# Optimization experiments

Measured on AMD Instinct MI355X. Metric: run time of the kernel, lower is better.

The kernel has to match this reference:

```python
import math
import jax, jax.numpy as jnp
import numpy as np

NUM_HEADS = 16
NUM_BUCKETS = 32
MAX_DISTANCE = 128
NEG_INF = -1e9
LN_EPS = 1e-5


def _rel_pos_bias(rab_emb, T):
    # buckets for relative position (i - j) clamped at 0, T5-style log buckets
    i = jnp.arange(T)[:, None]
    j = jnp.arange(T)[None, :]
    n = jnp.clip(i - j, 0, None)  # = -(mem - ctx), clamped min 0
    max_exact = NUM_BUCKETS // 2
    large = max_exact + (
        jnp.log(n.astype(jnp.float32) / max_exact + 1e-6)
        / math.log(MAX_DISTANCE / max_exact)
        * (NUM_BUCKETS - max_exact)
    ).astype(jnp.int32)
    large = jnp.minimum(large, NUM_BUCKETS - 1)
    buckets = jnp.where(n < max_exact, n, large)  # [T, T]
    return rab_emb[buckets].transpose(2, 0, 1)[None]  # [1, H, T, T]


def setup_inputs() -> dict:
    key = jax.random.key(0)
    ks = jax.random.split(key, 8)
    B, T, D = 2, 1024, 1024
    x = jax.random.normal(ks[0], (B, T, D), dtype=jnp.float32)
    # additive causal mask: 0 where allowed, -1e9 where blocked (code tests ==0 for allowed)
    causal_block = jnp.triu(jnp.ones((T, T), dtype=bool), k=1)
    attention_mask = jnp.where(causal_block, NEG_INF, 0.0).astype(jnp.float32)
    # key padding: second sequence has last 256 positions padded
    lengths = jnp.array([T, T - 256])
    key_padding_mask = jnp.arange(T)[None, :] >= lengths[:, None]  # True = pad
    s = 1.0 / math.sqrt(D)
    W_in = jax.random.normal(ks[1], (4 * D, D), dtype=jnp.float32) * s
    b_in = jax.random.normal(ks[2], (4 * D,), dtype=jnp.float32) * 0.02
    W_out = jax.random.normal(ks[3], (D, D), dtype=jnp.float32) * s
    b_out = jax.random.normal(ks[4], (D,), dtype=jnp.float32) * 0.02
    gamma = jnp.ones((D,), dtype=jnp.float32)
    beta = jnp.zeros((D,), dtype=jnp.float32)
    rab_emb = jax.random.normal(ks[5], (NUM_BUCKETS, NUM_HEADS), dtype=jnp.float32) * 0.02
    return {
        "x": x,
        "attention_mask": attention_mask,
        "key_padding_mask": key_padding_mask,
        "W_in": W_in,
        "b_in": b_in,
        "W_out": W_out,
        "b_out": b_out,
        "gamma": gamma,
        "beta": beta,
        "rab_emb": rab_emb,
    }


def reference(x, attention_mask, key_padding_mask, W_in, b_in, W_out, b_out, gamma, beta, rab_emb):
    B, T, D = x.shape
    H = NUM_HEADS
    hd = D // H
    alpha = hd ** (-0.5)

    h = jax.nn.silu(x @ W_in.T + b_in)  # [B, T, 4D]
    U, V, Q, K = jnp.split(h, 4, axis=-1)

    def heads(t):
        return t.reshape(B, T, H, hd).transpose(0, 2, 1, 3)  # [B, H, T, hd]

    Qh, Kh, Vh = heads(Q), heads(K), heads(V)

    rab = _rel_pos_bias(rab_emb, T)  # [1, H, T, T]
    logits = jnp.einsum("bhtd,bhsd->bhts", Qh, Kh) * alpha + rab + attention_mask[None, None]

    valid = (~key_padding_mask).astype(jnp.float32)[:, None, None, :]  # [B,1,1,T]
    allowed = (attention_mask == 0).astype(jnp.float32)[None, None] * valid  # [B,1,T,T] bcast
    # padded keys: torch masked_fill(-inf) then logits_safe -> -1e9
    logits = jnp.where(valid == 0, NEG_INF, logits)

    denom = jnp.clip(jnp.sum(allowed, axis=-1, keepdims=True), 1.0, None)
    attention = jax.nn.silu(logits) / denom  # pointwise SiLU attention, no softmax

    AV = jnp.einsum("bhts,bhsd->bthd", attention, Vh).reshape(B, T, D)

    mu = jnp.mean(AV, axis=-1, keepdims=True)
    var = jnp.var(AV, axis=-1, keepdims=True)
    normed = (AV - mu) / jnp.sqrt(var + LN_EPS) * gamma + beta

    y = (normed * U) @ W_out.T + b_out  # U_flat == U (head reshape round-trips)
    return x + y
```

## Files before the change

### kernel.cpp

```cpp
#include <hip/hip_runtime.h>
#include <stdint.h>

#define DEV static __device__ __forceinline__

typedef unsigned short u16;
typedef float floatx4 __attribute__((ext_vector_type(4)));
typedef short bf16x8 __attribute__((ext_vector_type(8)));

constexpr int Tn = 1024;
constexpr int Dn = 1024;
constexpr int Hn = 16;
constexpr int FD = 4096;

DEV float b2f(u16 u) { union { unsigned int i; float f; } v; v.i = ((unsigned int)u) << 16; return v.f; }
DEV u16 f2b(float f) {
  union { float f; unsigned int i; } v; v.f = f;
  unsigned int x = v.i;
  x += 0x7fffu + ((x >> 16) & 1u);
  return (u16)(x >> 16);
}

DEV void async16(const void* g, void* l) {
  __builtin_amdgcn_global_load_lds((const __attribute__((address_space(1))) void*)g,
                                   (__attribute__((address_space(3))) void*)l,
                                   16, 0, 0);
}

DEV bool is_bf16(const unsigned* gdet) { return gdet[0] == 0x3F803F80u; }
DEV int kp_mode(const unsigned* kp) {
  unsigned d511 = kp[511];
  if (d511 == 0x01010101u) return 1;
  unsigned d1023 = kp[1023];
  if (d1023 == 0x3F803F80u) return 2;
  unsigned d2047 = kp[2047];
  return (d2047 == 0x3F800000u) ? 3 : 0;
}
DEV int nchunks(int qt) { return (qt < 8) ? 1 : 2; }

__global__ void prep_all(const void* __restrict__ x, const void* __restrict__ wi,
                         const void* __restrict__ wo, u16* __restrict__ xb,
                         u16* __restrict__ wib, u16* __restrict__ wob,
                         const void* __restrict__ bi, const void* __restrict__ bo,
                         const void* __restrict__ ga, const void* __restrict__ be,
                         const void* __restrict__ kp, const void* __restrict__ rab,
                         float* __restrict__ smallf, float* __restrict__ biasG,
                         float* __restrict__ denomG, unsigned long long* __restrict__ kmaskG)
{
  const unsigned* gdet = (const unsigned*)ga;
  const int bid = blockIdx.x;
  const int tid = threadIdx.x;
  __shared__ unsigned char vb[1024];
  __shared__ int wtot[4];

  if (bid < 1792) {
    if (is_bf16(gdet)) return;
    int i0 = bid * 256 + tid;
#pragma unroll
    for (int k = 0; k < 4; k++) {
      int i = i0 + k * 458752;
      const void* src; u16* dst; int j;
      if (i < 524288)       { src = x;  dst = xb;  j = i; }
      else if (i < 1572864) { src = wi; dst = wib; j = i - 524288; }
      else                  { src = wo; dst = wob; j = i - 1572864; }
      float4 v = ((const float4*)src)[j];
      ushort4 o; o.x = f2b(v.x); o.y = f2b(v.y); o.z = f2b(v.z); o.w = f2b(v.w);
      ((ushort4*)dst)[j] = o;
    }
    return;
  }
  if (bid < 1794) {
    const int b = bid - 1792;
    const int mode = kp_mode((const unsigned*)kp);
    int vv[4];
    const int t0 = tid * 4;
#pragma unroll
    for (int i = 0; i < 4; i++) {
      int t = b * Tn + t0 + i;
      int pad;
      if (mode == 0)      pad = (((const int*)kp)[t] != 0);
      else if (mode == 1) pad = (((const unsigned char*)kp)[t] != 0);
      else if (mode == 2) pad = (((const u16*)kp)[t] != 0);
      else                pad = (((const float*)kp)[t] != 0.f);
      vv[i] = pad ? 0 : 1;
      vb[t0 + i] = (unsigned char)vv[i];
    }
    int p1 = vv[0], p2 = p1 + vv[1], p3 = p2 + vv[2], p4 = p3 + vv[3];
    const int lane = tid & 63, w = tid >> 6;
    int ws = p4;
#pragma unroll
    for (int off = 1; off < 64; off <<= 1) {
      int t = __shfl_up(ws, off, 64);
      if (lane >= off) ws += t;
    }
    if (lane == 63) wtot[w] = ws;
    __syncthreads();
    int base = 0;
    for (int j = 0; j < w; j++) base += wtot[j];
    int excl = base + ws - p4;
    int c1 = excl + p1, c2 = excl + p2, c3 = excl + p3, c4 = excl + p4;
    denomG[b * Tn + t0 + 0] = (float)(c1 < 1 ? 1 : c1);
    denomG[b * Tn + t0 + 1] = (float)(c2 < 1 ? 1 : c2);
    denomG[b * Tn + t0 + 2] = (float)(c3 < 1 ? 1 : c3);
    denomG[b * Tn + t0 + 3] = (float)(c4 < 1 ? 1 : c4);
    if (tid < 16) {
      unsigned long long m = 0;
      for (int j = 0; j < 64; j++) m |= (unsigned long long)vb[tid * 64 + j] << j;
      kmaskG[b * 16 + tid] = m;
    }
    return;
  }
  const bool fbf = is_bf16(gdet);
  for (int i = tid; i < 7168; i += 256) {
    const void* src; int j;
    if (i < 4096)      { src = bi; j = i; }
    else if (i < 5120) { src = bo; j = i - 4096; }
    else if (i < 6144) { src = ga; j = i - 5120; }
    else               { src = be; j = i - 6144; }
    smallf[i] = fbf ? b2f(((const u16*)src)[j]) : ((const float*)src)[j];
  }
  for (int i = tid; i < Hn * Tn; i += 256) {
    int hh = i >> 10, d = i & 1023;
    int bk;
    if (d < 16) bk = d;
    else {
      float lg = logf((float)d * 0.0625f + 1e-6f) / logf(8.f) * 16.f;
      bk = 16 + (int)lg;
      bk = bk < 31 ? bk : 31;
    }
    int j = bk * Hn + hh;
    biasG[i] = fbf ? b2f(((const u16*)rab)[j]) : ((const float*)rab)[j];
  }
}

template<int BM, int BN, int WR, int WC, int EPI>
__global__ __launch_bounds__(WR * WC * 64, 4)
void gemm_bt(const u16* __restrict__ Ac, const u16* __restrict__ Ar,
             const u16* __restrict__ Bc, const u16* __restrict__ Br,
             const float* __restrict__ biasf, const void* __restrict__ X,
             void* __restrict__ C, u16* __restrict__ VtG,
             const unsigned* __restrict__ gdet, int M, int N, int K)
{
  constexpr int NTH = WR * WC * 64;
  constexpr int MT = BM / (WR * 16);
  constexpr int NTT = BN / (WC * 16);
  __shared__ u16 As[2][BM * 64];
  __shared__ u16 Bs[2][BN * 64];
  const int fbf = is_bf16(gdet) ? 1 : 0;
  const u16* A  = fbf ? Ar : Ac;
  const u16* Bm = fbf ? Br : Bc;
  const int tid = threadIdx.x;
  const int lane = tid & 63;
  const int w = tid >> 6;
  const int wm = w / WC, wn = w % WC;
  const int q = lane >> 4, l16 = lane & 15;
  const int rowBase = blockIdx.y * BM;
  const int colBase = blockIdx.x * BN;
  const int nIter = K >> 6;

  floatx4 acc[MT][NTT];
#pragma unroll
  for (int i = 0; i < MT; i++)
#pragma unroll
    for (int j = 0; j < NTT; j++)
#pragma unroll
      for (int r = 0; r < 4; r++) acc[i][j][r] = 0.f;

  auto stage = [&](int buf, int kb) {
#pragma unroll
    for (int i = 0; i < BM * 8 / NTH; i++) {
      int c = i * NTH + tid;
      int row = c >> 3, cl = (c & 7) ^ (row & 7);
      async16(&A[(size_t)(rowBase + row) * K + kb + cl * 8], &As[buf][c * 8]);
    }
#pragma unroll
    for (int i = 0; i < BN * 8 / NTH; i++) {
      int c = i * NTH + tid;
      int row = c >> 3, cl = (c & 7) ^ (row & 7);
      async16(&Bm[(size_t)(colBase + row) * K + kb + cl * 8], &Bs[buf][c * 8]);
    }
  };

  stage(0, 0);
  __syncthreads();

  const int rsw = l16 & 7;
  for (int it = 0; it < nIter; it++) {
    const int cur = it & 1;
    if (it + 1 < nIter) stage(cur ^ 1, (it + 1) * 64);
#pragma unroll
    for (int ko = 0; ko < 2; ko++) {
      bf16x8 af[MT], bfr[NTT];
#pragma unroll
      for (int mt = 0; mt < MT; mt++) {
        int row = wm * (MT * 16) + mt * 16 + l16;
        af[mt] = *(const bf16x8*)&As[cur][(row * 8 + ((ko * 4 + q) ^ rsw)) * 8];
      }
#pragma unroll
      for (int nt = 0; nt < NTT; nt++) {
        int row = wn * (NTT * 16) + nt * 16 + l16;
        bfr[nt] = *(const bf16x8*)&Bs[cur][(row * 8 + ((ko * 4 + q) ^ rsw)) * 8];
      }
#pragma unroll
      for (int mt = 0; mt < MT; mt++)
#pragma unroll
        for (int nt = 0; nt < NTT; nt++)
          acc[mt][nt] = __builtin_amdgcn_mfma_f32_16x16x32_bf16(af[mt], bfr[nt], acc[mt][nt], 0, 0, 0);
    }
    __syncthreads();
  }

  const bool isV = (EPI == 0) && (colBase >= Dn) && (colBase < 2 * Dn);
#pragma unroll
  for (int mt = 0; mt < MT; mt++)
#pragma unroll
    for (int nt = 0; nt < NTT; nt++) {
      int col = colBase + wn * (NTT * 16) + nt * 16 + l16;
      float bcol = biasf[col];
      int row0 = rowBase + wm * (MT * 16) + mt * 16 + q * 4;
      if (EPI == 0) {
        u16 pr[4];
#pragma unroll
        for (int r = 0; r < 4; r++) {
          float v = acc[mt][nt][r] + bcol;
          v = v / (1.f + __expf(-v));
          pr[r] = f2b(v);
        }
        if (isV) {
          int d = col - Dn;
          u16* vp = &VtG[(((size_t)(row0 >> 10) * Hn + (d >> 6)) * 64 + (d & 63)) * Tn + (row0 & 1023)];
          *(uint2*)vp = make_uint2(pr[0] | ((unsigned)pr[1] << 16),
                                   pr[2] | ((unsigned)pr[3] << 16));
        } else {
#pragma unroll
          for (int r = 0; r < 4; r++)
            ((u16*)C)[(size_t)(row0 + r) * N + col] = pr[r];
        }
      } else {
#pragma unroll
        for (int r = 0; r < 4; r++) {
          size_t idx = (size_t)(row0 + r) * N + col;
          float v = acc[mt][nt][r] + bcol;
          if (fbf) {
            v += b2f(((const u16*)X)[idx]);
            ((u16*)C)[idx] = f2b(v);
          } else {
            v += ((const float*)X)[idx];
            ((float*)C)[idx] = v;
          }
        }
      }
    }
}

__global__ __launch_bounds__(256, 3)
void attn_kern(const u16* __restrict__ h, const u16* __restrict__ VtG,
               const float* __restrict__ biasG, const float* __restrict__ denomG,
               const unsigned long long* __restrict__ kmaskG,
               float* __restrict__ AV)
{
  __shared__ u16 QPs[4096];
  __shared__ u16 Ks[2][4096];
  __shared__ u16 Vs[2][4096];
  __shared__ float biasL[1024];
  const int tid = threadIdx.x;
  const int lane = tid & 63;
  const int w = tid >> 6;
  const int q = lane >> 4, l16 = lane & 15;

  int qt = 0, rem = blockIdx.x;
  for (;;) { int P = nchunks(qt); if (rem < P) break; rem -= P; qt++; }
  const int c = rem;
  const int P = nchunks(qt);
  const int n = qt + 1, cb = n / P, cr = n % P;
  const int kt0 = c * cb + (c < cr ? c : cr);
  const int kt1 = kt0 + cb + (c < cr ? 1 : 0);

  const int head = blockIdx.y, b = blockIdx.z;
  const u16* hb = h + (size_t)b * Tn * FD;
  const u16* vtb = VtG + ((size_t)(b * Hn + head)) * 64 * Tn;

#pragma unroll
  for (int i = 0; i < 2; i++) {
    int s = i * 256 + tid;
    int row = s >> 3, dc = (s & 7) ^ (row & 7);
    async16(&hb[(size_t)(qt * 64 + row) * FD + 2048 + head * 64 + dc * 8], &QPs[s * 8]);
    async16(&hb[(size_t)(kt0 * 64 + row) * FD + 3072 + head * 64 + dc * 8], &Ks[0][s * 8]);
    async16(&vtb[(size_t)row * Tn + kt0 * 64 + dc * 8], &Vs[0][s * 8]);
  }
  async16(&biasG[head * Tn + tid * 4], &biasL[tid * 4]);
  __syncthreads();

  const int sw0 = q ^ (l16 & 7);
  const int qrow = w * 16 + l16;
  bf16x8 bq0 = *(const bf16x8*)&QPs[(qrow * 8 + sw0) * 8];
  bf16x8 bq1 = *(const bf16x8*)&QPs[(qrow * 8 + (sw0 ^ 4)) * 8];
  const float dinv = 1.f / denomG[b * Tn + qt * 64 + qrow];

  floatx4 o[4];
#pragma unroll
  for (int nt = 0; nt < 4; nt++)
#pragma unroll
    for (int r = 0; r < 4; r++) o[nt][r] = 0.f;

  int buf = 0;
  for (int kt = kt0; kt < kt1; kt++) {
    if (kt + 1 < kt1) {
      int nb = buf ^ 1;
      int krow = (kt + 1) * 64;
#pragma unroll
      for (int i = 0; i < 2; i++) {
        int s = i * 256 + tid;
        int row = s >> 3, dc = (s & 7) ^ (row & 7);
        async16(&hb[(size_t)(krow + row) * FD + 3072 + head * 64 + dc * 8], &Ks[nb][s * 8]);
        async16(&vtb[(size_t)row * Tn + krow + dc * 8], &Vs[nb][s * 8]);
      }
    }
    const unsigned long long km = kmaskG[b * 16 + kt];
    const int dq = (qt - kt) * 64 + qrow;
#pragma unroll
    for (int st = 0; st < 4; st++) {
      int rk = (st * 16 + l16) * 8;
      bf16x8 ak0 = *(const bf16x8*)&Ks[buf][(rk + sw0) * 8];
      bf16x8 ak1 = *(const bf16x8*)&Ks[buf][(rk + (sw0 ^ 4)) * 8];
      floatx4 sT;
#pragma unroll
      for (int r = 0; r < 4; r++) sT[r] = 0.f;
      sT = __builtin_amdgcn_mfma_f32_16x16x32_bf16(ak0, bq0, sT, 0, 0, 0);
      sT = __builtin_amdgcn_mfma_f32_16x16x32_bf16(ak1, bq1, sT, 0, 0, 0);
      unsigned mb = (unsigned)(km >> (st * 16 + q * 4)) & 0xFu;
      u16 pr[4];
#pragma unroll
      for (int r = 0; r < 4; r++) {
        int delta = dq - (st * 16 + q * 4 + r);
        float p = 0.f;
        if (((mb >> r) & 1u) && delta >= 0) {
          float xv = sT[r] * 0.125f + biasL[delta];
          p = xv * dinv / (1.f + __expf(-xv));
        }
        pr[r] = f2b(p);
      }
      unsigned lo = pr[0] | ((unsigned)pr[1] << 16);
      unsigned hi = pr[2] | ((unsigned)pr[3] << 16);
      int cch = (st * 2 + (q >> 1)) ^ (l16 & 7);
      *(uint2*)&QPs[w * 1024 + l16 * 64 + cch * 8 + (q & 1) * 4] = make_uint2(lo, hi);
    }
    int rp = w * 1024 + l16 * 64;
    bf16x8 ap0 = *(const bf16x8*)&QPs[rp + sw0 * 8];
    bf16x8 ap1 = *(const bf16x8*)&QPs[rp + (sw0 ^ 4) * 8];
#pragma unroll
    for (int nt = 0; nt < 4; nt++) {
      int rv = (nt * 16 + l16) * 8;
      bf16x8 bv0 = *(const bf16x8*)&Vs[buf][(rv + sw0) * 8];
      bf16x8 bv1 = *(const bf16x8*)&Vs[buf][(rv + (sw0 ^ 4)) * 8];
      o[nt] = __builtin_amdgcn_mfma_f32_16x16x32_bf16(ap0, bv0, o[nt], 0, 0, 0);
      o[nt] = __builtin_amdgcn_mfma_f32_16x16x32_bf16(ap1, bv1, o[nt], 0, 0, 0);
    }
    if (kt + 1 < kt1) __syncthreads();
    buf ^= 1;
  }

  float* avp = AV + (size_t)c * 2097152
             + ((size_t)b * Tn + qt * 64 + w * 16 + q * 4) * Dn + head * 64;
#pragma unroll
  for (int nt = 0; nt < 4; nt++)
#pragma unroll
    for (int r = 0; r < 4; r++)
      avp[(size_t)r * Dn + nt * 16 + l16] = o[nt][r];
}

__global__ __launch_bounds__(256)
void ln_mul(const float* __restrict__ AV, const u16* __restrict__ h,
            const float* __restrict__ gam, const float* __restrict__ bet,
            u16* __restrict__ z)
{
  struct alignas(8) U4 { u16 a, b, c, d; };
  const int row = blockIdx.x;
  const int tid = threadIdx.x;
  const int P = nchunks(row >> 6 & 15);
  float4 v = ((const float4*)(AV + (size_t)row * Dn))[tid];
  if (P > 1) {
    float4 p = ((const float4*)(AV + 2097152 + (size_t)row * Dn))[tid];
    v.x += p.x; v.y += p.y; v.z += p.z; v.w += p.w;
  }
  float s  = v.x + v.y + v.z + v.w;
  float s2 = v.x * v.x + v.y * v.y + v.z * v.z + v.w * v.w;
#pragma unroll
  for (int off = 32; off > 0; off >>= 1) {
    s  += __shfl_down(s, off, 64);
    s2 += __shfl_down(s2, off, 64);
  }
  __shared__ float red[8];
  const int lane = tid & 63, w = tid >> 6;
  if (lane == 0) { red[w] = s; red[4 + w] = s2; }
  __syncthreads();
  const float su = red[0] + red[1] + red[2] + red[3];
  const float sq = red[4] + red[5] + red[6] + red[7];
  const float mu = su * (1.f / 1024.f);
  const float var = sq * (1.f / 1024.f) - mu * mu;
  const float rstd = rsqrtf(var + 1e-5f);

  const U4 uu = ((const U4*)(h + (size_t)row * FD))[tid];
  const float4 g4 = ((const float4*)gam)[tid];
  const float4 b4 = ((const float4*)bet)[tid];
  float r0 = ((v.x - mu) * rstd * g4.x + b4.x) * b2f(uu.a);
  float r1 = ((v.y - mu) * rstd * g4.y + b4.y) * b2f(uu.b);
  float r2 = ((v.z - mu) * rstd * g4.z + b4.z) * b2f(uu.c);
  float r3 = ((v.w - mu) * rstd * g4.w + b4.w) * b2f(uu.d);
  U4 outv; outv.a = f2b(r0); outv.b = f2b(r1); outv.c = f2b(r2); outv.d = f2b(r3);
  ((U4*)(z + (size_t)row * Dn))[tid] = outv;
}

extern "C" void kernel_launch(void* const* d_in, const int* in_sizes, int n_in,
                              void* d_out, int out_size, void* d_ws, size_t ws_size,
                              hipStream_t stream)
{
  const void* x     = d_in[0];
  const void* kp    = d_in[2];
  const void* W_in  = d_in[3];
  const void* b_in  = d_in[4];
  const void* W_out = d_in[5];
  const void* b_out = d_in[6];
  const void* gamma = d_in[7];
  const void* beta  = d_in[8];
  const void* rab   = d_in[9];
  const unsigned* gdet = (const unsigned*)gamma;

  char* ws = (char*)d_ws;
  u16*   h     = (u16*)(ws);
  float* AV    = (float*)(ws + 16777216);
  u16*   z     = (u16*)(ws + 41943040);
  u16*   xb    = (u16*)(ws + 46137344);
  u16*   Wib   = (u16*)(ws + 50331648);
  u16*   Wob   = (u16*)(ws + 58720256);
  u16*   VtG   = (u16*)(ws + 60817408);
  float* smallf= (float*)(ws + 65011712);
  float* biasG = (float*)(ws + 65040384);
  float* denom = (float*)(ws + 65105920);
  unsigned long long* kmask = (unsigned long long*)(ws + 65114112);

  prep_all<<<1795, 256, 0, stream>>>(x, W_in, W_out, xb, Wib, Wob,
                                     b_in, b_out, gamma, beta, kp, rab,
                                     smallf, biasG, denom, kmask);
  gemm_bt<128, 128, 4, 2, 0><<<dim3(32, 16, 1), dim3(512), 0, stream>>>(
      xb, (const u16*)x, Wib, (const u16*)W_in, smallf, nullptr,
      h, VtG, gdet, 2048, 4096, 1024);
  attn_kern<<<dim3(24, 16, 2), dim3(256), 0, stream>>>(h, VtG, biasG, denom, kmask, AV);
  ln_mul<<<2048, 256, 0, stream>>>(AV, h, smallf + 5120, smallf + 6144, z);
  gemm_bt<64, 64, 4, 2, 1><<<dim3(16, 32, 1), dim3(512), 0, stream>>>(
      z, z, Wob, (const u16*)W_out, smallf + 4096, x, d_out, nullptr,
      gdet, 2048, 1024, 1024);
}
```

Baseline: 183.1 us.

## Split attention keys three ways, single-buffer K/V, add constant-bias fast path

Causal key tiles are now split across up to three chunks for late query tiles instead of two, and the LayerNorm kernel sums the third partial. K/V shared memory drops from double to single buffering so the kernel can target four blocks per SM, with extra barriers around each tile load. Tiles whose key mask is all zero skip their compute. Tiles far enough from the diagonal and fully unmasked use one constant relative-position bias with no per-element mask checks. Losing double buffering exposes global load latency that the higher occupancy is meant to hide.

```diff
diff --git a/kernel.cpp b/kernel.cpp
--- a/kernel.cpp
+++ b/kernel.cpp
@@ -35,7 +35,7 @@
   unsigned d2047 = kp[2047];
   return (d2047 == 0x3F800000u) ? 3 : 0;
 }
-DEV int nchunks(int qt) { return (qt < 8) ? 1 : 2; }
+DEV int nchunks(int qt) { return (qt < 6) ? 1 : ((qt < 12) ? 2 : 3); }
 
 __global__ void prep_all(const void* __restrict__ x, const void* __restrict__ wi,
                          const void* __restrict__ wo, u16* __restrict__ xb,
@@ -252,15 +252,16 @@
     }
 }
 
-__global__ __launch_bounds__(256, 3)
+__global__ __launch_bounds__(256, 4)
 void attn_kern(const u16* __restrict__ h, const u16* __restrict__ VtG,
                const float* __restrict__ biasG, const float* __restrict__ denomG,
                const unsigned long long* __restrict__ kmaskG,
                float* __restrict__ AV)
 {
-  __shared__ u16 QPs[4096];
-  __shared__ u16 Ks[2][4096];
-  __shared__ u16 Vs[2][4096];
+  __shared__ u16 Qs[4096];
+  __shared__ u16 Ks[4096];
+  __shared__ u16 Vs[4096];
+  __shared__ u16 Ps[4096];
   __shared__ float biasL[1024];
   const int tid = threadIdx.x;
   const int lane = tid & 63;
@@ -283,18 +284,19 @@
   for (int i = 0; i < 2; i++) {
     int s = i * 256 + tid;
     int row = s >> 3, dc = (s & 7) ^ (row & 7);
-    async16(&hb[(size_t)(qt * 64 + row) * FD + 2048 + head * 64 + dc * 8], &QPs[s * 8]);
-    async16(&hb[(size_t)(kt0 * 64 + row) * FD + 3072 + head * 64 + dc * 8], &Ks[0][s * 8]);
-    async16(&vtb[(size_t)row * Tn + kt0 * 64 + dc * 8], &Vs[0][s * 8]);
+    async16(&hb[(size_t)(qt * 64 + row) * FD + 2048 + head * 64 + dc * 8], &Qs[s * 8]);
+    async16(&hb[(size_t)(kt0 * 64 + row) * FD + 3072 + head * 64 + dc * 8], &Ks[s * 8]);
+    async16(&vtb[(size_t)row * Tn + kt0 * 64 + dc * 8], &Vs[s * 8]);
   }
   async16(&biasG[head * Tn + tid * 4], &biasL[tid * 4]);
   __syncthreads();
 
   const int sw0 = q ^ (l16 & 7);
   const int qrow = w * 16 + l16;
-  bf16x8 bq0 = *(const bf16x8*)&QPs[(qrow * 8 + sw0) * 8];
-  bf16x8 bq1 = *(const bf16x8*)&QPs[(qrow * 8 + (sw0 ^ 4)) * 8];
+  bf16x8 bq0 = *(const bf16x8*)&Qs[(qrow * 8 + sw0) * 8];
+  bf16x8 bq1 = *(const bf16x8*)&Qs[(qrow * 8 + (sw0 ^ 4)) * 8];
   const float dinv = 1.f / denomG[b * Tn + qt * 64 + qrow];
+  const float cb31 = biasL[512];
 
   floatx4 o[4];
 #pragma unroll
@@ -302,61 +304,70 @@
 #pragma unroll
     for (int r = 0; r < 4; r++) o[nt][r] = 0.f;
 
-  int buf = 0;
   for (int kt = kt0; kt < kt1; kt++) {
+    const unsigned long long km = kmaskG[b * 16 + kt];
+    if (km != 0ull) {
+      const bool fastT = (qt - kt >= 3) && (km == ~0ull);
+      const int dq = (qt - kt) * 64 + qrow;
+#pragma unroll
+      for (int st = 0; st < 4; st++) {
+        int rk = (st * 16 + l16) * 8;
+        bf16x8 ak0 = *(const bf16x8*)&Ks[(rk + sw0) * 8];
+        bf16x8 ak1 = *(const bf16x8*)&Ks[(rk + (sw0 ^ 4)) * 8];
+        floatx4 sT;
+#pragma unroll
+        for (int r = 0; r < 4; r++) sT[r] = 0.f;
+        sT = __builtin_amdgcn_mfma_f32_16x16x32_bf16(ak0, bq0, sT, 0, 0, 0);
+        sT = __builtin_amdgcn_mfma_f32_16x16x32_bf16(ak1, bq1, sT, 0, 0, 0);
+        u16 pr[4];
+        if (fastT) {
+#pragma unroll
+          for (int r = 0; r < 4; r++) {
+            float xv = sT[r] * 0.125f + cb31;
+            float p = xv * dinv / (1.f + __expf(-xv));
+            pr[r] = f2b(p);
+          }
+        } else {
+          unsigned mb = (unsigned)(km >> (st * 16 + q * 4)) & 0xFu;
+#pragma unroll
+          for (int r = 0; r < 4; r++) {
+            int delta = dq - (st * 16 + q * 4 + r);
+            float p = 0.f;
+            if (((mb >> r) & 1u) && delta >= 0) {
+              float xv = sT[r] * 0.125f + biasL[delta];
+              p = xv * dinv / (1.f + __expf(-xv));
+            }
+            pr[r] = f2b(p);
+          }
+        }
+        unsigned lo = pr[0] | ((unsigned)pr[1] << 16);
+        unsigned hi = pr[2] | ((unsigned)pr[3] << 16);
+        int cch = (st * 2 + (q >> 1)) ^ (l16 & 7);
+        *(uint2*)&Ps[w * 1024 + l16 * 64 + cch * 8 + (q & 1) * 4] = make_uint2(lo, hi);
+      }
+      int rp = w * 1024 + l16 * 64;
+      bf16x8 ap0 = *(const bf16x8*)&Ps[rp + sw0 * 8];
+      bf16x8 ap1 = *(const bf16x8*)&Ps[rp + (sw0 ^ 4) * 8];
+#pragma unroll
+      for (int nt = 0; nt < 4; nt++) {
+        int rv = (nt * 16 + l16) * 8;
+        bf16x8 bv0 = *(const bf16x8*)&Vs[(rv + sw0) * 8];
+        bf16x8 bv1 = *(const bf16x8*)&Vs[(rv + (sw0 ^ 4)) * 8];
+        o[nt] = __builtin_amdgcn_mfma_f32_16x16x32_bf16(ap0, bv0, o[nt], 0, 0, 0);
+        o[nt] = __builtin_amdgcn_mfma_f32_16x16x32_bf16(ap1, bv1, o[nt], 0, 0, 0);
+      }
+    }
     if (kt + 1 < kt1) {
-      int nb = buf ^ 1;
-      int krow = (kt + 1) * 64;
+      __syncthreads();
 #pragma unroll
       for (int i = 0; i < 2; i++) {
         int s = i * 256 + tid;
         int row = s >> 3, dc = (s & 7) ^ (row & 7);
-        async16(&hb[(size_t)(krow + row) * FD + 3072 + head * 64 + dc * 8], &Ks[nb][s * 8]);
-        async16(&vtb[(size_t)row * Tn + krow + dc * 8], &Vs[nb][s * 8]);
-      }
-    }
-    const unsigned long long km = kmaskG[b * 16 + kt];
-    const int dq = (qt - kt) * 64 + qrow;
-#pragma unroll
-    for (int st = 0; st < 4; st++) {
-      int rk = (st * 16 + l16) * 8;
-      bf16x8 ak0 = *(const bf16x8*)&Ks[buf][(rk + sw0) * 8];
-      bf16x8 ak1 = *(const bf16x8*)&Ks[buf][(rk + (sw0 ^ 4)) * 8];
-      floatx4 sT;
-#pragma unroll
-      for (int r = 0; r < 4; r++) sT[r] = 0.f;
-      sT = __builtin_amdgcn_mfma_f32_16x16x32_bf16(ak0, bq0, sT, 0, 0, 0);
-      sT = __builtin_amdgcn_mfma_f32_16x16x32_bf16(ak1, bq1, sT, 0, 0, 0);
-      unsigned mb = (unsigned)(km >> (st * 16 + q * 4)) & 0xFu;
-      u16 pr[4];
-#pragma unroll
-      for (int r = 0; r < 4; r++) {
-        int delta = dq - (st * 16 + q * 4 + r);
-        float p = 0.f;
-        if (((mb >> r) & 1u) && delta >= 0) {
-          float xv = sT[r] * 0.125f + biasL[delta];
-          p = xv * dinv / (1.f + __expf(-xv));
-        }
-        pr[r] = f2b(p);
-      }
-      unsigned lo = pr[0] | ((unsigned)pr[1] << 16);
-      unsigned hi = pr[2] | ((unsigned)pr[3] << 16);
-      int cch = (st * 2 + (q >> 1)) ^ (l16 & 7);
-      *(uint2*)&QPs[w * 1024 + l16 * 64 + cch * 8 + (q & 1) * 4] = make_uint2(lo, hi);
-    }
-    int rp = w * 1024 + l16 * 64;
-    bf16x8 ap0 = *(const bf16x8*)&QPs[rp + sw0 * 8];
-    bf16x8 ap1 = *(const bf16x8*)&QPs[rp + (sw0 ^ 4) * 8];
-#pragma unroll
-    for (int nt = 0; nt < 4; nt++) {
-      int rv = (nt * 16 + l16) * 8;
-      bf16x8 bv0 = *(const bf16x8*)&Vs[buf][(rv + sw0) * 8];
-      bf16x8 bv1 = *(const bf16x8*)&Vs[buf][(rv + (sw0 ^ 4)) * 8];
-      o[nt] = __builtin_amdgcn_mfma_f32_16x16x32_bf16(ap0, bv0, o[nt], 0, 0, 0);
-      o[nt] = __builtin_amdgcn_mfma_f32_16x16x32_bf16(ap1, bv1, o[nt], 0, 0, 0);
-    }
-    if (kt + 1 < kt1) __syncthreads();
-    buf ^= 1;
+        async16(&hb[(size_t)((kt + 1) * 64 + row) * FD + 3072 + head * 64 + dc * 8], &Ks[s * 8]);
+        async16(&vtb[(size_t)row * Tn + (kt + 1) * 64 + dc * 8], &Vs[s * 8]);
+      }
+      __syncthreads();
+    }
   }
 
   float* avp = AV + (size_t)c * 2097152
@@ -380,6 +391,10 @@
   float4 v = ((const float4*)(AV + (size_t)row * Dn))[tid];
   if (P > 1) {
     float4 p = ((const float4*)(AV + 2097152 + (size_t)row * Dn))[tid];
+    v.x += p.x; v.y += p.y; v.z += p.z; v.w += p.w;
+  }
+  if (P > 2) {
+    float4 p = ((const float4*)(AV + 4194304 + (size_t)row * Dn))[tid];
     v.x += p.x; v.y += p.y; v.z += p.z; v.w += p.w;
   }
   float s  = v.x + v.y + v.z + v.w;
@@ -444,7 +459,7 @@
   gemm_bt<128, 128, 4, 2, 0><<<dim3(32, 16, 1), dim3(512), 0, stream>>>(
       xb, (const u16*)x, Wib, (const u16*)W_in, smallf, nullptr,
       h, VtG, gdet, 2048, 4096, 1024);
-  attn_kern<<<dim3(24, 16, 2), dim3(256), 0, stream>>>(h, VtG, biasG, denom, kmask, AV);
+  attn_kern<<<dim3(30, 16, 2), dim3(256), 0, stream>>>(h, VtG, biasG, denom, kmask, AV);
   ln_mul<<<2048, 256, 0, stream>>>(AV, h, smallf + 5120, smallf + 6144, z);
   gemm_bt<64, 64, 4, 2, 1><<<dim3(16, 32, 1), dim3(512), 0, stream>>>(
       z, z, Wob, (const u16*)W_out, smallf + 4096, x, d_out, nullptr,
```

Result: no change. 182.8 us (-0.2%).
